# Optimization experiments

Hardware: AMD Instinct MI355X
Metric: run time of the kernel (lower is better)

The kernel has to match this reference:

```python
import jax, jax.numpy as jnp
import numpy as np

EPS = 1e-5  # clamp epsilon; also used to fill the background slab (as in the torch code)


def setup_inputs() -> dict:
    key = jax.random.key(0)
    # smoothed voxel occupancies in [0, 1): [B, D, H, W]
    voxels = jax.random.uniform(key, (16, 128, 128, 128), dtype=jnp.float32)
    return {"voxels": voxels}


def reference(voxels) -> jnp.ndarray:
    # voxels: [B, D, H, W] occupancy grid; D is the ray/depth axis.
    B, D, H, W = voxels.shape
    o = jnp.clip(voxels, EPS, 1.0 - EPS)
    log_free = jnp.log(1.0 - o)          # log prob ray passes each cell
    log_occ = jnp.log(o)                 # log prob ray terminates at each cell
    # cumulative transmittance in log space along depth
    cum_free = jnp.cumsum(log_free, axis=1)            # [B, D, H, W]
    eps_slab = jnp.full((B, 1, H, W), EPS, dtype=voxels.dtype)
    r1 = jnp.concatenate([eps_slab, cum_free], axis=1)  # [B, D+1, H, W]
    r2 = jnp.concatenate([log_occ, eps_slab], axis=1)   # [B, D+1, H, W]
    probs = jnp.exp(r1 + r2)                             # ray termination probs
    # drop background cell, project along depth, flip vertically
    return jnp.flip(probs[:, :-1].sum(axis=1), axis=1)   # [B, H, W]
```

## Files before the change

kernel.cpp:

```cpp
#include <hip/hip_runtime.h>


#define EPS 1e-5f
#define EXP_EPS 1.0000100000500002f

#define B_ 16
#define D_ 128
#define H_ 128
#define W_ 128

__device__ __forceinline__ float clampo(float v) {
    return fminf(fmaxf(v, EPS), 1.0f - EPS);
}

__global__ __launch_bounds__(128) void ray_term_kernel(const float* __restrict__ vox,
                                                       float* __restrict__ out) {
    const int w4 = threadIdx.x;
    const int h  = blockIdx.x * blockDim.y + threadIdx.y;
    const int b  = blockIdx.y;

    const float4* __restrict__ src =
        (const float4*)(vox + ((size_t)b * D_ * H_ + (size_t)h) * W_) + w4;
    const int dstride = H_ * W_ / 4;

    float4 v0 = src[0];
    float o0 = clampo(v0.x), o1 = clampo(v0.y), o2 = clampo(v0.z), o3 = clampo(v0.w);
    float a0 = o0 * EXP_EPS, a1 = o1 * EXP_EPS, a2 = o2 * EXP_EPS, a3 = o3 * EXP_EPS;
    float T0 = 1.0f - o0, T1 = 1.0f - o1, T2 = 1.0f - o2, T3 = 1.0f - o3;

    #pragma unroll 8
    for (int d = 1; d < D_; ++d) {
        float4 v = src[(size_t)d * dstride];
        o0 = clampo(v.x); o1 = clampo(v.y); o2 = clampo(v.z); o3 = clampo(v.w);
        a0 = fmaf(o0, T0, a0); T0 *= (1.0f - o0);
        a1 = fmaf(o1, T1, a1); T1 *= (1.0f - o1);
        a2 = fmaf(o2, T2, a2); T2 *= (1.0f - o2);
        a3 = fmaf(o3, T3, a3); T3 *= (1.0f - o3);
    }

    float* __restrict__ dst =
        out + ((size_t)b * H_ + (size_t)(H_ - 1 - h)) * W_ + 4 * w4;
    *(float4*)dst = make_float4(a0, a1, a2, a3);
}

extern "C" void kernel_launch(void* const* d_in, const int* in_sizes, int n_in,
                              void* d_out, int out_size, void* d_ws, size_t ws_size,
                              hipStream_t stream) {
    const float* vox = (const float*)d_in[0];
    float* out = (float*)d_out;
    dim3 block(32, 4, 1);
    dim3 grid(H_ / 4, B_, 1);
    ray_term_kernel<<<grid, block, 0, stream>>>(vox, out);
}
```

Before: 184.2 us.

## Split depth scan into four chunks per wave and combine with shuffles

Each ray's depth accumulation is split into four chunks handled by different lane groups within a wavefront. Partial transmittance products and accumulations are merged with cross-lane shuffles, and block and grid shapes are enlarged to match. This raises the number of threads in flight and shortens each serial load chain, to better hide memory latency on a bandwidth-bound scan. It adds shuffle overhead and slightly changes floating-point association.

```diff
diff --git a/kernel.cpp b/kernel.cpp
--- a/kernel.cpp
+++ b/kernel.cpp
@@ -8,39 +8,67 @@
 #define D_ 128
 #define H_ 128
 #define W_ 128
+#define CH_ 4
+#define CD_ (D_ / CH_)
 
 __device__ __forceinline__ float clampo(float v) {
     return fminf(fmaxf(v, EPS), 1.0f - EPS);
 }
 
-__global__ __launch_bounds__(128) void ray_term_kernel(const float* __restrict__ vox,
-                                                       float* __restrict__ out) {
-    const int w4 = threadIdx.x;
-    const int h  = blockIdx.x * blockDim.y + threadIdx.y;
-    const int b  = blockIdx.y;
+__global__ __launch_bounds__(256, 4) void ray_term_kernel(const float* __restrict__ vox,
+                                                          float* __restrict__ out) {
+    const int lane  = threadIdx.x;
+    const int wv    = threadIdx.y;
+    const int chunk = lane >> 4;
+    const int w4    = (lane & 15) + 16 * (wv & 1);
+    const int h     = blockIdx.x * 2 + (wv >> 1);
+    const int b     = blockIdx.y;
 
     const float4* __restrict__ src =
-        (const float4*)(vox + ((size_t)b * D_ * H_ + (size_t)h) * W_) + w4;
+        (const float4*)(vox + (((size_t)b * D_ + (size_t)chunk * CD_) * H_ + h) * W_) + w4;
     const int dstride = H_ * W_ / 4;
 
+    const float s = (chunk == 0) ? EXP_EPS : 1.0f;
     float4 v0 = src[0];
     float o0 = clampo(v0.x), o1 = clampo(v0.y), o2 = clampo(v0.z), o3 = clampo(v0.w);
-    float a0 = o0 * EXP_EPS, a1 = o1 * EXP_EPS, a2 = o2 * EXP_EPS, a3 = o3 * EXP_EPS;
-    float T0 = 1.0f - o0, T1 = 1.0f - o1, T2 = 1.0f - o2, T3 = 1.0f - o3;
+    float a0 = o0 * s, a1 = o1 * s, a2 = o2 * s, a3 = o3 * s;
+    float t0 = 1.0f - o0, t1 = 1.0f - o1, t2 = 1.0f - o2, t3 = 1.0f - o3;
 
     #pragma unroll 8
-    for (int d = 1; d < D_; ++d) {
+    for (int d = 1; d < CD_; ++d) {
         float4 v = src[(size_t)d * dstride];
         o0 = clampo(v.x); o1 = clampo(v.y); o2 = clampo(v.z); o3 = clampo(v.w);
-        a0 = fmaf(o0, T0, a0); T0 *= (1.0f - o0);
-        a1 = fmaf(o1, T1, a1); T1 *= (1.0f - o1);
-        a2 = fmaf(o2, T2, a2); T2 *= (1.0f - o2);
-        a3 = fmaf(o3, T3, a3); T3 *= (1.0f - o3);
+        a0 = fmaf(o0, t0, a0); t0 *= (1.0f - o0);
+        a1 = fmaf(o1, t1, a1); t1 *= (1.0f - o1);
+        a2 = fmaf(o2, t2, a2); t2 *= (1.0f - o2);
+        a3 = fmaf(o3, t3, a3); t3 *= (1.0f - o3);
     }
 
-    float* __restrict__ dst =
-        out + ((size_t)b * H_ + (size_t)(H_ - 1 - h)) * W_ + 4 * w4;
-    *(float4*)dst = make_float4(a0, a1, a2, a3);
+    const int base = lane & 15;
+    float u0, u1, u2, P;
+#define COMBINE(T, A)                                  \
+    u0 = __shfl((T), base + 0, 64);                    \
+    u1 = __shfl((T), base + 16, 64);                   \
+    u2 = __shfl((T), base + 32, 64);                   \
+    P = 1.0f;                                          \
+    if (chunk > 0) P = u0;                             \
+    if (chunk > 1) P *= u1;                            \
+    if (chunk > 2) P *= u2;                            \
+    (A) *= P;                                          \
+    (A) += __shfl_xor((A), 16, 64);                    \
+    (A) += __shfl_xor((A), 32, 64);
+
+    COMBINE(t0, a0)
+    COMBINE(t1, a1)
+    COMBINE(t2, a2)
+    COMBINE(t3, a3)
+#undef COMBINE
+
+    if (chunk == 0) {
+        float* __restrict__ dst =
+            out + ((size_t)b * H_ + (size_t)(H_ - 1 - h)) * W_ + 4 * w4;
+        *(float4*)dst = make_float4(a0, a1, a2, a3);
+    }
 }
 
 extern "C" void kernel_launch(void* const* d_in, const int* in_sizes, int n_in,
@@ -48,7 +76,7 @@
                               hipStream_t stream) {
     const float* vox = (const float*)d_in[0];
     float* out = (float*)d_out;
-    dim3 block(32, 4, 1);
-    dim3 grid(H_ / 4, B_, 1);
+    dim3 block(64, 4, 1);
+    dim3 grid(H_ / 2, B_, 1);
     ray_term_kernel<<<grid, block, 0, stream>>>(vox, out);
 }
```

Measured after the change: 185.7 us. Within noise of the previous version (+0.9%).
